# Optimization experiments

Hardware: AMD Instinct MI355X
Metric: run time of the kernel (lower is better)

The kernel has to match this reference:

```python
import jax, jax.numpy as jnp
import numpy as np

H_IMG, W_IMG = 160, 160
C1, C2, HEADS, NHOPS = 128, 256, 8, 2
N_NODES = H_IMG * W_IMG


def build_edges(H, W):
    # 3x3 neighborhood (excl. self) + skip edges (i+2,j),(i,j+2); self loops added once
    node = (np.arange(H)[:, None] * W + np.arange(W)[None, :])
    offsets = [(di, dj) for di in (-1, 0, 1) for dj in (-1, 0, 1) if (di, dj) != (0, 0)] + [(2, 0), (0, 2)]
    srcs, dsts = [], []
    for di, dj in offsets:
        i0, i1 = max(0, -di), H - max(0, di)
        j0, j1 = max(0, -dj), W - max(0, dj)
        srcs.append(node[i0:i1, j0:j1].ravel())
        dsts.append(node[i0 + di:i1 + di, j0 + dj:j1 + dj].ravel())
    n = np.arange(H * W)
    srcs.append(n); dsts.append(n)
    return (np.concatenate(srcs).astype(np.int32), np.concatenate(dsts).astype(np.int32))


def setup_inputs() -> dict:
    key = jax.random.key(0)
    ks = jax.random.split(key, 16)
    s = 0.05
    src_np, dst_np = build_edges(H_IMG, W_IMG)
    d = C2 // HEADS
    return {
        "x": jax.random.normal(ks[0], (1, C1, H_IMG, W_IMG), jnp.float32),
        "w_id": jax.random.normal(ks[1], (C2, C1), jnp.float32) * s,
        "w_in": jax.random.normal(ks[2], (C2, C1), jnp.float32) * s,
        "w_gat": jax.random.normal(ks[3], (NHOPS, C2, C2), jnp.float32) * s,
        "a_src": jax.random.normal(ks[4], (NHOPS, HEADS, d), jnp.float32) * s,
        "a_dst": jax.random.normal(ks[5], (NHOPS, HEADS, d), jnp.float32) * s,
        "gat_bias": jax.random.normal(ks[6], (NHOPS, C2), jnp.float32) * s,
        "bn_gamma": jax.random.uniform(ks[7], (NHOPS, C2), jnp.float32, 0.5, 1.5),
        "bn_beta": jax.random.normal(ks[8], (NHOPS, C2), jnp.float32) * s,
        "bn_mean": jax.random.normal(ks[9], (NHOPS, C2), jnp.float32) * s,
        "bn_var": jax.random.uniform(ks[10], (NHOPS, C2), jnp.float32, 0.5, 1.5),
        "w_out": jax.random.normal(ks[11], (C2, C2), jnp.float32) * s,
        "se_w1": jax.random.normal(ks[12], (C2 // 4, C2), jnp.float32) * s,
        "se_b1": jax.random.normal(ks[13], (C2 // 4,), jnp.float32) * s,
        "se_w2": jax.random.normal(ks[14], (C2, C2 // 4), jnp.float32) * s,
        "se_b2": jax.random.normal(ks[15], (C2,), jnp.float32) * s,
        "src": jnp.asarray(src_np),
        "dst": jnp.asarray(dst_np),
    }


def _gat(x, W, a_s, a_d, b, src, dst, N):
    heads, d = a_s.shape
    h = (x @ W.T).reshape(N, heads, d)                      # [N,H,D]
    al_s = jnp.einsum('nhd,hd->nh', h, a_s)                 # [N,H]
    al_d = jnp.einsum('nhd,hd->nh', h, a_d)
    e = jax.nn.leaky_relu(al_s[src] + al_d[dst], 0.2)       # [E,H]
    emax = jax.lax.stop_gradient(jax.ops.segment_max(e, dst, num_segments=N))
    ee = jnp.exp(e - emax[dst])
    denom = jax.ops.segment_sum(ee, dst, num_segments=N)
    alpha = ee / (denom[dst] + 1e-16)                       # segment softmax over incoming edges
    out = jax.ops.segment_sum(h[src] * alpha[..., None], dst, num_segments=N)
    return out.reshape(N, heads * d) + b


def _forward(x, w_id, w_in, w_gat, a_src, a_dst, gat_bias, bn_gamma, bn_beta,
             bn_mean, bn_var, w_out, se_w1, se_b1, se_w2, se_b2, src, dst):
    identity = jnp.einsum('bchw,oc->bohw', x, w_id)
    h = jnp.einsum('bchw,oc->bohw', x, w_in)
    B, C, H, W = h.shape
    N = B * H * W
    xf = h.transpose(0, 2, 3, 1).reshape(N, C)
    for l in range(NHOPS):
        res = xf
        g = _gat(xf, w_gat[l], a_src[l], a_dst[l], gat_bias[l], src, dst, N)
        g = (g - bn_mean[l]) * (bn_gamma[l] * jax.lax.rsqrt(bn_var[l] + 1e-5)) + bn_beta[l]
        xf = jax.nn.relu(g) + res
    y = xf.reshape(B, H, W, C).transpose(0, 3, 1, 2)
    y = jnp.einsum('bchw,oc->bohw', y, w_out)
    # SE block
    w = y.mean(axis=(2, 3))                                 # [B,C]
    w = jax.nn.relu(w @ se_w1.T + se_b1)
    w = jax.nn.sigmoid(w @ se_w2.T + se_b2)
    y = y * w[:, :, None, None]
    return y + identity


def reference(x, w_id, w_in, w_gat, a_src, a_dst, gat_bias, bn_gamma, bn_beta,
              bn_mean, bn_var, w_out, se_w1, se_b1, se_w2, se_b2, src, dst):
    return _forward(x, w_id, w_in, w_gat, a_src, a_dst, gat_bias, bn_gamma, bn_beta,
                    bn_mean, bn_var, w_out, se_w1, se_b1, se_w2, se_b2, src, dst)
```

## Files before the change

kernel.cpp:

```cpp
#include <hip/hip_runtime.h>

#define NN 25600
#define HH 160
#define WW 160
#define C2 256

#define B_WIN   0
#define B_WID   32768
#define B_WGAT  65536
#define B_WOUT  196608
#define B_WEND  262144

#define C_BNA   0
#define C_BNB   512
#define C_ASRC  1024
#define C_ADST  1536
#define C_SEW1  2048
#define C_SEB1  18432
#define C_SEW2  18496
#define C_SEB2  34880
#define C_END   35136

typedef __attribute__((ext_vector_type(8))) short bfrag;
typedef __attribute__((ext_vector_type(4))) float ffrag;

__device__ __forceinline__ float b2f(unsigned short u) {
    union { unsigned int ui; float f; } v; v.ui = ((unsigned int)u) << 16; return v.f;
}
__device__ __forceinline__ unsigned short f2b(float f) {
    union { float f; unsigned int u; } v; v.f = f;
    unsigned int u = v.u;
    unsigned int r = (u + 0x7FFFu + ((u >> 16) & 1u)) >> 16;
    return (unsigned short)r;
}
__device__ __forceinline__ float lo16f(unsigned int w) {
    union { unsigned int ui; float f; } v; v.ui = w << 16; return v.f;
}
__device__ __forceinline__ float hi16f(unsigned int w) {
    union { unsigned int ui; float f; } v; v.ui = w & 0xFFFF0000u; return v.f;
}
__device__ __forceinline__ bool probe_f32(const unsigned short* __restrict__ x) {
    int l = threadIdx.x & 63;
    bool wild = false;
#pragma unroll
    for (int i = 0; i < 8; ++i) {
        float v = b2f(x[l * 8 + i]);
        wild |= !(fabsf(v) < 1e6f);
    }
    return __any(wild);
}
__device__ __forceinline__ float ldf(const void* p, long i, bool f32) {
    return f32 ? ((const float*)p)[i] : b2f(((const unsigned short*)p)[i]);
}

__global__ __launch_bounds__(256) void prep_kernel(
    const unsigned short* __restrict__ xp,
    const void* pwin, const void* pwid, const void* pwgat, const void* pwout,
    const void* pasrc, const void* padst, const void* pgbias,
    const void* pbng, const void* pbnb, const void* pbnm, const void* pbnv,
    const void* psew1, const void* pseb1, const void* psew2, const void* pseb2,
    unsigned short* __restrict__ wb, float* __restrict__ cvt,
    float* __restrict__ means, unsigned short* __restrict__ xT)
{
    __shared__ unsigned short T[64 * 136];
    const bool f32 = probe_f32(xp);
    const int tid = threadIdx.x;
    const int bid = blockIdx.x;
    const int gid = bid * 256 + tid;
    const int stride = gridDim.x * 256;

    if (bid == 0) means[tid] = 0.f;

    for (int i = gid; i < B_WEND; i += stride) {
        const void* s; int o;
        if      (i < B_WID)   { s = pwin;  o = i - B_WIN; }
        else if (i < B_WGAT)  { s = pwid;  o = i - B_WID; }
        else if (i < B_WOUT)  { s = pwgat; o = i - B_WGAT; }
        else                  { s = pwout; o = i - B_WOUT; }
        wb[i] = f32 ? f2b(((const float*)s)[o]) : ((const unsigned short*)s)[o];
    }
    for (int i = gid; i < 512; i += stride) {
        float sc = ldf(pbng, i, f32) * rsqrtf(ldf(pbnv, i, f32) + 1e-5f);
        cvt[C_BNA + i] = sc;
        cvt[C_BNB + i] = (ldf(pgbias, i, f32) - ldf(pbnm, i, f32)) * sc + ldf(pbnb, i, f32);
        cvt[C_ASRC + i] = ldf(pasrc, i, f32);
        cvt[C_ADST + i] = ldf(padst, i, f32);
    }
    for (int i = gid; i < 16384; i += stride) {
        cvt[C_SEW1 + i] = ldf(psew1, i, f32);
        cvt[C_SEW2 + i] = ldf(psew2, i, f32);
    }
    for (int i = gid; i < 64; i += stride)  cvt[C_SEB1 + i] = ldf(pseb1, i, f32);
    for (int i = gid; i < 256; i += stride) cvt[C_SEB2 + i] = ldf(pseb2, i, f32);

    {
        const int n0 = bid * 64;
        const int nl = tid & 63;
#pragma unroll
        for (int i = 0; i < 32; ++i) {
            int c = i * 4 + (tid >> 6);
            long idx = (long)c * NN + n0 + nl;
            T[nl * 136 + c] = f32 ? f2b(((const float*)xp)[idx]) : xp[idx];
        }
        __syncthreads();
#pragma unroll
        for (int i = 0; i < 4; ++i) {
            int n = tid >> 2, c0 = (tid & 3) * 32 + i * 8;
            uint4 v = *(const uint4*)&T[n * 136 + c0];
            *(uint4*)(xT + (long)(n0 + n) * 128 + c0) = v;
        }
    }
}

struct SmemG2 { unsigned short As[128*40], Bi[64*40], Bd[64*40]; };
struct SmemG  { unsigned short As[128*40], Bs[64*40]; };
struct SmemC  { unsigned short Cs[128*72]; };
union  SmemX2 { SmemG2 s; SmemC c; };
union  SmemNN { SmemG s; SmemC c; };

__global__ __launch_bounds__(256) void mfma_gemm_x2_kernel(
    const unsigned short* __restrict__ A16,
    const unsigned short* __restrict__ Wi16,
    const unsigned short* __restrict__ Wd16,
    unsigned short* __restrict__ xf16,
    unsigned short* __restrict__ idb16)
{
    __shared__ SmemX2 sm;
    const int tid = threadIdx.x;
    const int m0 = blockIdx.x * 128, o0 = blockIdx.y * 64;
    const int lane = tid & 63, wv = tid >> 6;
    const int wm = wv >> 1, wn = wv & 1;
    const int lr = lane & 15, quad = lane >> 4;

    ffrag ai[4][2], ad[4][2];
#pragma unroll
    for (int mt = 0; mt < 4; ++mt)
#pragma unroll
        for (int nt = 0; nt < 2; ++nt) { ai[mt][nt] = (ffrag){0,0,0,0}; ad[mt][nt] = (ffrag){0,0,0,0}; }

    for (int k0 = 0; k0 < 128; k0 += 32) {
#pragma unroll
        for (int c = tid; c < 512; c += 256) {
            int row = c >> 2, q = c & 3;
            uint4 v = *(const uint4*)(A16 + (long)(m0 + row) * 128 + k0 + q * 8);
            *(uint4*)&sm.s.As[row * 40 + q * 8] = v;
        }
        {
            int row = tid >> 2, q = tid & 3;
            uint4 vi = *(const uint4*)(Wi16 + (long)(o0 + row) * 128 + k0 + q * 8);
            uint4 vd = *(const uint4*)(Wd16 + (long)(o0 + row) * 128 + k0 + q * 8);
            *(uint4*)&sm.s.Bi[row * 40 + q * 8] = vi;
            *(uint4*)&sm.s.Bd[row * 40 + q * 8] = vd;
        }
        __syncthreads();
        bfrag a[4], bi[2], bd[2];
#pragma unroll
        for (int mt = 0; mt < 4; ++mt)
            a[mt] = *(const bfrag*)&sm.s.As[(wm * 64 + mt * 16 + lr) * 40 + quad * 8];
#pragma unroll
        for (int nt = 0; nt < 2; ++nt) {
            bi[nt] = *(const bfrag*)&sm.s.Bi[(wn * 32 + nt * 16 + lr) * 40 + quad * 8];
            bd[nt] = *(const bfrag*)&sm.s.Bd[(wn * 32 + nt * 16 + lr) * 40 + quad * 8];
        }
#pragma unroll
        for (int mt = 0; mt < 4; ++mt)
#pragma unroll
            for (int nt = 0; nt < 2; ++nt) {
                ai[mt][nt] = __builtin_amdgcn_mfma_f32_16x16x32_bf16(a[mt], bi[nt], ai[mt][nt], 0, 0, 0);
                ad[mt][nt] = __builtin_amdgcn_mfma_f32_16x16x32_bf16(a[mt], bd[nt], ad[mt][nt], 0, 0, 0);
            }
        __syncthreads();
    }
#pragma unroll
    for (int mt = 0; mt < 4; ++mt)
#pragma unroll
        for (int nt = 0; nt < 2; ++nt)
#pragma unroll
            for (int r = 0; r < 4; ++r)
                sm.c.Cs[(wm * 64 + mt * 16 + quad * 4 + r) * 72 + wn * 32 + nt * 16 + lr] = f2b(ai[mt][nt][r]);
    __syncthreads();
#pragma unroll
    for (int it = 0; it < 4; ++it) {
        int e = it * 256 + tid;
        int row = e >> 3, c8 = (e & 7) * 8;
        *(uint4*)(xf16 + (long)(m0 + row) * C2 + o0 + c8) = *(const uint4*)&sm.c.Cs[row * 72 + c8];
    }
    __syncthreads();
#pragma unroll
    for (int mt = 0; mt < 4; ++mt)
#pragma unroll
        for (int nt = 0; nt < 2; ++nt)
#pragma unroll
            for (int r = 0; r < 4; ++r)
                sm.c.Cs[(wm * 64 + mt * 16 + quad * 4 + r) * 72 + wn * 32 + nt * 16 + lr] = f2b(ad[mt][nt][r]);
    __syncthreads();
#pragma unroll
    for (int it = 0; it < 4; ++it) {
        int e = it * 256 + tid;
        int row = e >> 3, c8 = (e & 7) * 8;
        *(uint4*)(idb16 + (long)(m0 + row) * C2 + o0 + c8) = *(const uint4*)&sm.c.Cs[row * 72 + c8];
    }
}

__global__ __launch_bounds__(256) void mfma_gemm_nn_kernel(
    const unsigned short* __restrict__ A16,
    const unsigned short* __restrict__ W16,
    unsigned short* __restrict__ C16,
    const float* __restrict__ asrc, const float* __restrict__ adst,
    float* __restrict__ al_s, float* __restrict__ al_d,
    float* __restrict__ means,
    int mode)
{
    __shared__ SmemNN sm;
    const int tid = threadIdx.x;
    const int m0 = blockIdx.x * 128, o0 = blockIdx.y * 64;
    const int lane = tid & 63, wv = tid >> 6;
    const int wm = wv >> 1, wn = wv & 1;
    const int lr = lane & 15, quad = lane >> 4;

    ffrag acc[4][2];
#pragma unroll
    for (int mt = 0; mt < 4; ++mt)
#pragma unroll
        for (int nt = 0; nt < 2; ++nt) acc[mt][nt] = (ffrag){0,0,0,0};

    for (int k0 = 0; k0 < 256; k0 += 32) {
#pragma unroll
        for (int c = tid; c < 512; c += 256) {
            int row = c >> 2, q = c & 3;
            uint4 v = *(const uint4*)(A16 + (long)(m0 + row) * 256 + k0 + q * 8);
            *(uint4*)&sm.s.As[row * 40 + q * 8] = v;
        }
        {
            int row = tid >> 2, q = tid & 3;
            uint4 v = *(const uint4*)(W16 + (long)(o0 + row) * 256 + k0 + q * 8);
            *(uint4*)&sm.s.Bs[row * 40 + q * 8] = v;
        }
        __syncthreads();
        bfrag a[4], b[2];
#pragma unroll
        for (int mt = 0; mt < 4; ++mt)
            a[mt] = *(const bfrag*)&sm.s.As[(wm * 64 + mt * 16 + lr) * 40 + quad * 8];
#pragma unroll
        for (int nt = 0; nt < 2; ++nt)
            b[nt] = *(const bfrag*)&sm.s.Bs[(wn * 32 + nt * 16 + lr) * 40 + quad * 8];
#pragma unroll
        for (int mt = 0; mt < 4; ++mt)
#pragma unroll
            for (int nt = 0; nt < 2; ++nt)
                acc[mt][nt] = __builtin_amdgcn_mfma_f32_16x16x32_bf16(a[mt], b[nt], acc[mt][nt], 0, 0, 0);
        __syncthreads();
    }
#pragma unroll
    for (int mt = 0; mt < 4; ++mt)
#pragma unroll
        for (int nt = 0; nt < 2; ++nt)
#pragma unroll
            for (int r = 0; r < 4; ++r)
                sm.c.Cs[(wm * 64 + mt * 16 + quad * 4 + r) * 72 + wn * 32 + nt * 16 + lr] = f2b(acc[mt][nt][r]);
    __syncthreads();
#pragma unroll
    for (int it = 0; it < 4; ++it) {
        int e = it * 256 + tid;
        int row = e >> 3, c8 = (e & 7) * 8;
        *(uint4*)(C16 + (long)(m0 + row) * C2 + o0 + c8) = *(const uint4*)&sm.c.Cs[row * 72 + c8];
    }
    if (mode == 1) {
        const int head = blockIdx.y * 2 + wn;
        const float as0 = asrc[head * 32 + lr], as1 = asrc[head * 32 + 16 + lr];
        const float ad0 = adst[head * 32 + lr], ad1 = adst[head * 32 + 16 + lr];
#pragma unroll
        for (int mt = 0; mt < 4; ++mt)
#pragma unroll
            for (int r = 0; r < 4; ++r) {
                float ps = acc[mt][0][r] * as0 + acc[mt][1][r] * as1;
                float pd = acc[mt][0][r] * ad0 + acc[mt][1][r] * ad1;
#pragma unroll
                for (int sh = 1; sh < 16; sh <<= 1) {
                    ps += __shfl_xor(ps, sh);
                    pd += __shfl_xor(pd, sh);
                }
                if (lr == 0) {
                    int m = m0 + wm * 64 + mt * 16 + quad * 4 + r;
                    al_s[m * 8 + head] = ps;
                    al_d[m * 8 + head] = pd;
                }
            }
    } else if (mode == 2) {
#pragma unroll
        for (int nt = 0; nt < 2; ++nt) {
            float p = 0.f;
#pragma unroll
            for (int mt = 0; mt < 4; ++mt)
#pragma unroll
                for (int r = 0; r < 4; ++r) p += acc[mt][nt][r];
            p += __shfl_xor(p, 16);
            p += __shfl_xor(p, 32);
            if (quad == 0) atomicAdd(&means[o0 + wn * 32 + nt * 16 + lr], p);
        }
    }
}

__global__ __launch_bounds__(256) void aggregate_kernel(
    const unsigned short* __restrict__ h16,
    const float* __restrict__ al_s,
    const float* __restrict__ al_d,
    const float* __restrict__ bnA,
    const float* __restrict__ bnB,
    unsigned short* __restrict__ xf16)
{
    const int SI[11] = { 1, 1, 1, 0, 0, -1, -1, -1, -2,  0, 0};
    const int SJ[11] = { 1, 0,-1, 1,-1,  1,  0, -1,  0, -2, 0};
    __shared__ float es[8][11][8];
    __shared__ float alpha[8][11][8];

    const int t = threadIdx.x;
    const int ln = t >> 5;
    const int l = t & 31;
    const int n = blockIdx.x * 8 + ln;
    const int i = n / WW, j = n % WW;

    for (int idx = t; idx < 704; idx += 256) {
        int lln = idx / 88, rem = idx - lln * 88;
        int k = rem >> 3, hh = rem & 7;
        int nn2 = blockIdx.x * 8 + lln;
        int ii = nn2 / WW, jj = nn2 - ii * WW;
        int si = ii + SI[k], sj = jj + SJ[k];
        bool okk = (si >= 0) & (si < HH) & (sj >= 0) & (sj < WW);
        es[lln][k][hh] = okk ? al_s[(si * WW + sj) * 8 + hh] : -1e30f;
    }
    __syncthreads();

    if (l < 8) {
        const int hd = l;
        const float ald = al_d[n * 8 + hd];
        float e[11];
        float mx = -1e30f;
#pragma unroll
        for (int k = 0; k < 11; ++k) {
            float v = es[ln][k][hd] + ald;
            v = v > 0.f ? v : 0.2f * v;
            e[k] = v;
            mx = fmaxf(mx, v);
        }
        float denom = 0.f;
#pragma unroll
        for (int k = 0; k < 11; ++k) {
            float p = __expf(e[k] - mx);
            e[k] = p;
            denom += p;
        }
        const float inv = 1.f / (denom + 1e-16f);
#pragma unroll
        for (int k = 0; k < 11; ++k) alpha[ln][k][hd] = e[k] * inv;
    }
    __syncthreads();

    const int c8 = l * 8;
    const int hd = l >> 2;
    int srcn[11];
#pragma unroll
    for (int k = 0; k < 11; ++k) {
        int si = i + SI[k], sj = j + SJ[k];
        bool ok = (si >= 0) & (si < HH) & (sj >= 0) & (sj < WW);
        srcn[k] = ok ? si * WW + sj : n;
    }
    float a0=0.f,a1=0.f,a2=0.f,a3=0.f,a4=0.f,a5=0.f,a6=0.f,a7=0.f;
#pragma unroll
    for (int k = 0; k < 11; ++k) {
        float al = alpha[ln][k][hd];
        uint4 hv = *(const uint4*)(h16 + (long)srcn[k] * C2 + c8);
        a0 += al * lo16f(hv.x); a1 += al * hi16f(hv.x);
        a2 += al * lo16f(hv.y); a3 += al * hi16f(hv.y);
        a4 += al * lo16f(hv.z); a5 += al * hi16f(hv.z);
        a6 += al * lo16f(hv.w); a7 += al * hi16f(hv.w);
    }
    float acc8[8] = {a0,a1,a2,a3,a4,a5,a6,a7};
    uint4 rv = *(const uint4*)(xf16 + (long)n * C2 + c8);
    float res[8] = {lo16f(rv.x),hi16f(rv.x),lo16f(rv.y),hi16f(rv.y),
                    lo16f(rv.z),hi16f(rv.z),lo16f(rv.w),hi16f(rv.w)};
    float out[8];
#pragma unroll
    for (int q = 0; q < 8; ++q) {
        int c = c8 + q;
        float g = acc8[q] * bnA[c] + bnB[c];
        out[q] = fmaxf(g, 0.f) + res[q];
    }
    ushort4 o16a, o16b;
    o16a.x = f2b(out[0]); o16a.y = f2b(out[1]); o16a.z = f2b(out[2]); o16a.w = f2b(out[3]);
    o16b.x = f2b(out[4]); o16b.y = f2b(out[5]); o16b.z = f2b(out[6]); o16b.w = f2b(out[7]);
    *(ushort4*)(xf16 + (long)n * C2 + c8)     = o16a;
    *(ushort4*)(xf16 + (long)n * C2 + c8 + 4) = o16b;
}

__global__ __launch_bounds__(256) void final_kernel(
    const unsigned short* __restrict__ x_probe,
    const unsigned short* __restrict__ y16,
    const unsigned short* __restrict__ idb16,
    const float* __restrict__ means,
    const float* __restrict__ cvt,
    void* __restrict__ outp)
{
    __shared__ float T[64][65];
    __shared__ float mv[256];
    __shared__ float hv[64];
    __shared__ float sv[64];
    const bool f32o = probe_f32(x_probe);
    const int t = threadIdx.x;
    const int n0 = blockIdx.x * 64, c0 = blockIdx.y * 64;

    mv[t] = means[t] * (1.0f / 25600.0f);
    __syncthreads();
    if (t < 64) {
        const float* w1 = cvt + C_SEW1 + t * 256;
        float s = cvt[C_SEB1 + t];
        for (int cc = 0; cc < 256; cc += 4) {
            float4 wv = *(const float4*)(w1 + cc);
            s += wv.x * mv[cc] + wv.y * mv[cc+1] + wv.z * mv[cc+2] + wv.w * mv[cc+3];
        }
        hv[t] = fmaxf(s, 0.f);
    }
    __syncthreads();
    if (t < 64) {
        const int c = c0 + t;
        const float* w2 = cvt + C_SEW2 + c * 64;
        float s = cvt[C_SEB2 + c];
        for (int k = 0; k < 64; k += 4) {
            float4 wv = *(const float4*)(w2 + k);
            s += wv.x * hv[k] + wv.y * hv[k+1] + wv.z * hv[k+2] + wv.w * hv[k+3];
        }
        sv[t] = 1.0f / (1.0f + __expf(-s));
    }
    __syncthreads();
#pragma unroll
    for (int it = 0; it < 16; ++it) {
        int e = t + it * 256;
        int nn = e >> 6, cc = e & 63;
        long idx = (long)(n0 + nn) * C2 + c0 + cc;
        T[cc][nn] = b2f(y16[idx]) * sv[cc] + b2f(idb16[idx]);
    }
    __syncthreads();
#pragma unroll
    for (int it = 0; it < 16; ++it) {
        int e = t + it * 256;
        int cc = e >> 6, nn = e & 63;
        long idx = (long)(c0 + cc) * NN + n0 + nn;
        float v = T[cc][nn];
        if (f32o) ((float*)outp)[idx] = v;
        else      ((unsigned short*)outp)[idx] = f2b(v);
    }
}

extern "C" void kernel_launch(void* const* d_in, const int* in_sizes, int n_in,
                              void* d_out, int out_size, void* d_ws, size_t ws_size,
                              hipStream_t stream) {
    float* ws = (float*)d_ws;
    float* cvt   = ws;
    float* means = ws + 35200;
    float* als   = means + 256;
    float* ald   = als + 204800;
    unsigned short* wb16  = (unsigned short*)(ald + 204800);
    unsigned short* xT16  = wb16 + B_WEND;
    unsigned short* xf16  = xT16 + NN * 128;
    unsigned short* h16   = xf16 + NN * 256;
    unsigned short* idb16 = h16 + NN * 256;

    const unsigned short* xp = (const unsigned short*)d_in[0];

    dim3 b256(256);
    dim3 gmfma(NN / 128, C2 / 64);
    dim3 gfin(NN / 64, C2 / 64);

    prep_kernel<<<400, b256, 0, stream>>>(
        xp, d_in[2], d_in[1], d_in[3], d_in[11],
        d_in[4], d_in[5], d_in[6], d_in[7], d_in[8], d_in[9], d_in[10],
        d_in[12], d_in[13], d_in[14], d_in[15],
        wb16, cvt, means, xT16);

    mfma_gemm_x2_kernel<<<gmfma, b256, 0, stream>>>(
        xT16, wb16 + B_WIN, wb16 + B_WID, xf16, idb16);

    for (int l = 0; l < 2; ++l) {
        mfma_gemm_nn_kernel<<<gmfma, b256, 0, stream>>>(
            xf16, wb16 + B_WGAT + l * 65536, h16,
            cvt + C_ASRC + l * 256, cvt + C_ADST + l * 256, als, ald, nullptr, 1);
        aggregate_kernel<<<NN / 8, b256, 0, stream>>>(h16, als, ald,
            cvt + C_BNA + l * 256, cvt + C_BNB + l * 256, xf16);
    }

    mfma_gemm_nn_kernel<<<gmfma, b256, 0, stream>>>(
        xf16, wb16 + B_WOUT, h16, nullptr, nullptr, nullptr, nullptr, means, 2);
    final_kernel<<<gfin, b256, 0, stream>>>(xp, h16, idb16, means, cvt, d_out);
}
```

Baseline: 240.2 us.

## Fuse GAT aggregation into the following GEMM's A-tile producer

Removes the separate aggregate kernel. The next GEMM (next hop's W_gat or w_out) now computes the softmax attention weights and the neighbour-weighted sum plus BN/ReLU/residual on the fly, building its A tile in shared memory per K-slice. It also widens the GEMM N-tile from 64 to 128 so each aggregated A row is reused across more outputs. It double-buffers the h and alpha buffers to avoid read/write hazards. Each hop saves a full round trip of the xf activation through memory and one launch, but the gather and softmax are redone for each of the two N-blocks and may hurt GEMM throughput and occupancy.

```diff
diff --git a/kernel.cpp b/kernel.cpp
--- a/kernel.cpp
+++ b/kernel.cpp
@@ -113,10 +113,8 @@
 }
 
 struct SmemG2 { unsigned short As[128*40], Bi[64*40], Bd[64*40]; };
-struct SmemG  { unsigned short As[128*40], Bs[64*40]; };
-struct SmemC  { unsigned short Cs[128*72]; };
-union  SmemX2 { SmemG2 s; SmemC c; };
-union  SmemNN { SmemG s; SmemC c; };
+struct SmemC2 { unsigned short Cs[128*72]; };
+union  SmemX2 { SmemG2 s; SmemC2 c; };
 
 __global__ __launch_bounds__(256) void mfma_gemm_x2_kernel(
     const unsigned short* __restrict__ A16,
@@ -142,15 +140,15 @@
 #pragma unroll
         for (int c = tid; c < 512; c += 256) {
             int row = c >> 2, q = c & 3;
-            uint4 v = *(const uint4*)(A16 + (long)(m0 + row) * 128 + k0 + q * 8);
-            *(uint4*)&sm.s.As[row * 40 + q * 8] = v;
+            *(uint4*)&sm.s.As[row * 40 + q * 8] =
+                *(const uint4*)(A16 + (long)(m0 + row) * 128 + k0 + q * 8);
         }
         {
             int row = tid >> 2, q = tid & 3;
-            uint4 vi = *(const uint4*)(Wi16 + (long)(o0 + row) * 128 + k0 + q * 8);
-            uint4 vd = *(const uint4*)(Wd16 + (long)(o0 + row) * 128 + k0 + q * 8);
-            *(uint4*)&sm.s.Bi[row * 40 + q * 8] = vi;
-            *(uint4*)&sm.s.Bd[row * 40 + q * 8] = vd;
+            *(uint4*)&sm.s.Bi[row * 40 + q * 8] =
+                *(const uint4*)(Wi16 + (long)(o0 + row) * 128 + k0 + q * 8);
+            *(uint4*)&sm.s.Bd[row * 40 + q * 8] =
+                *(const uint4*)(Wd16 + (long)(o0 + row) * 128 + k0 + q * 8);
         }
         __syncthreads();
         bfrag a[4], bi[2], bd[2];
@@ -202,93 +200,184 @@
     }
 }
 
-__global__ __launch_bounds__(256) void mfma_gemm_nn_kernel(
-    const unsigned short* __restrict__ A16,
+__global__ __launch_bounds__(256) void gemm_hop_kernel(
+    const unsigned short* __restrict__ Ap,
+    const unsigned short* __restrict__ hsrc,
+    const float* __restrict__ alsA, const float* __restrict__ aldA,
+    const unsigned short* __restrict__ xfold,
+    unsigned short* __restrict__ xfout,
+    const float* __restrict__ bnA, const float* __restrict__ bnB,
     const unsigned short* __restrict__ W16,
     unsigned short* __restrict__ C16,
     const float* __restrict__ asrc, const float* __restrict__ adst,
-    float* __restrict__ al_s, float* __restrict__ al_d,
+    float* __restrict__ al_sO, float* __restrict__ al_dO,
     float* __restrict__ means,
-    int mode)
+    int aggA, int epi)
 {
-    __shared__ SmemNN sm;
+    __shared__ union {
+        struct { unsigned short As[128*40], Bs[128*40]; float alpha[128][11]; } s;
+        unsigned short Cs[128*136];
+    } sm;
+    const int SI[11] = { 1, 1, 1, 0, 0, -1, -1, -1, -2,  0, 0};
+    const int SJ[11] = { 1, 0,-1, 1,-1,  1,  0, -1,  0, -2, 0};
     const int tid = threadIdx.x;
-    const int m0 = blockIdx.x * 128, o0 = blockIdx.y * 64;
+    const int m0 = blockIdx.x * 128, o0 = blockIdx.y * 128;
     const int lane = tid & 63, wv = tid >> 6;
     const int wm = wv >> 1, wn = wv & 1;
     const int lr = lane & 15, quad = lane >> 4;
 
-    ffrag acc[4][2];
+    ffrag acc[4][4];
 #pragma unroll
     for (int mt = 0; mt < 4; ++mt)
 #pragma unroll
-        for (int nt = 0; nt < 2; ++nt) acc[mt][nt] = (ffrag){0,0,0,0};
+        for (int nt = 0; nt < 4; ++nt) acc[mt][nt] = (ffrag){0,0,0,0};
 
     for (int k0 = 0; k0 < 256; k0 += 32) {
 #pragma unroll
         for (int c = tid; c < 512; c += 256) {
             int row = c >> 2, q = c & 3;
-            uint4 v = *(const uint4*)(A16 + (long)(m0 + row) * 256 + k0 + q * 8);
-            *(uint4*)&sm.s.As[row * 40 + q * 8] = v;
-        }
-        {
-            int row = tid >> 2, q = tid & 3;
-            uint4 v = *(const uint4*)(W16 + (long)(o0 + row) * 256 + k0 + q * 8);
-            *(uint4*)&sm.s.Bs[row * 40 + q * 8] = v;
+            *(uint4*)&sm.s.Bs[row * 40 + q * 8] =
+                *(const uint4*)(W16 + (long)(o0 + row) * 256 + k0 + q * 8);
+        }
+        if (aggA) {
+            if (tid < 128) {
+                const int head = k0 >> 5;
+                const int m = m0 + tid;
+                const int i2 = m / WW, j2 = m - i2 * WW;
+                const float ald = aldA[m * 8 + head];
+                float e[11]; float mx = -1e30f;
+#pragma unroll
+                for (int k = 0; k < 11; ++k) {
+                    int si = i2 + SI[k], sj = j2 + SJ[k];
+                    bool ok = (si >= 0) & (si < HH) & (sj >= 0) & (sj < WW);
+                    float v = ok ? alsA[(si * WW + sj) * 8 + head] + ald : -1e30f;
+                    v = v > 0.f ? v : 0.2f * v;
+                    e[k] = v; mx = fmaxf(mx, v);
+                }
+                float den = 0.f;
+#pragma unroll
+                for (int k = 0; k < 11; ++k) { float p = __expf(e[k] - mx); e[k] = p; den += p; }
+                const float inv = 1.f / (den + 1e-16f);
+#pragma unroll
+                for (int k = 0; k < 11; ++k) sm.s.alpha[tid][k] = e[k] * inv;
+            }
+        } else {
+#pragma unroll
+            for (int c = tid; c < 512; c += 256) {
+                int row = c >> 2, q = c & 3;
+                *(uint4*)&sm.s.As[row * 40 + q * 8] =
+                    *(const uint4*)(Ap + (long)(m0 + row) * 256 + k0 + q * 8);
+            }
         }
         __syncthreads();
-        bfrag a[4], b[2];
+        if (aggA) {
+            const int ml = tid >> 1, half = tid & 1;
+            const int m = m0 + ml;
+            const int i2 = m / WW, j2 = m - i2 * WW;
+            const int cb = k0 + half * 16;
+            float a16[16];
+#pragma unroll
+            for (int q = 0; q < 16; ++q) a16[q] = 0.f;
+#pragma unroll
+            for (int k = 0; k < 11; ++k) {
+                float al = sm.s.alpha[ml][k];
+                int si = i2 + SI[k], sj = j2 + SJ[k];
+                bool ok = (si >= 0) & (si < HH) & (sj >= 0) & (sj < WW);
+                long srcn = ok ? (long)(si * WW + sj) : (long)m;
+                uint4 v0 = *(const uint4*)(hsrc + srcn * C2 + cb);
+                uint4 v1 = *(const uint4*)(hsrc + srcn * C2 + cb + 8);
+                a16[0]  += al * lo16f(v0.x); a16[1]  += al * hi16f(v0.x);
+                a16[2]  += al * lo16f(v0.y); a16[3]  += al * hi16f(v0.y);
+                a16[4]  += al * lo16f(v0.z); a16[5]  += al * hi16f(v0.z);
+                a16[6]  += al * lo16f(v0.w); a16[7]  += al * hi16f(v0.w);
+                a16[8]  += al * lo16f(v1.x); a16[9]  += al * hi16f(v1.x);
+                a16[10] += al * lo16f(v1.y); a16[11] += al * hi16f(v1.y);
+                a16[12] += al * lo16f(v1.z); a16[13] += al * hi16f(v1.z);
+                a16[14] += al * lo16f(v1.w); a16[15] += al * hi16f(v1.w);
+            }
+            uint4 r0 = *(const uint4*)(xfold + (long)m * C2 + cb);
+            uint4 r1 = *(const uint4*)(xfold + (long)m * C2 + cb + 8);
+            float res[16] = {lo16f(r0.x),hi16f(r0.x),lo16f(r0.y),hi16f(r0.y),
+                             lo16f(r0.z),hi16f(r0.z),lo16f(r0.w),hi16f(r0.w),
+                             lo16f(r1.x),hi16f(r1.x),lo16f(r1.y),hi16f(r1.y),
+                             lo16f(r1.z),hi16f(r1.z),lo16f(r1.w),hi16f(r1.w)};
+            unsigned int w[8];
+#pragma unroll
+            for (int q = 0; q < 8; ++q) {
+                int c0i = cb + q * 2;
+                float g0 = a16[q*2]   * bnA[c0i]     + bnB[c0i];
+                float g1 = a16[q*2+1] * bnA[c0i + 1] + bnB[c0i + 1];
+                g0 = fmaxf(g0, 0.f) + res[q*2];
+                g1 = fmaxf(g1, 0.f) + res[q*2+1];
+                w[q] = (unsigned int)f2b(g0) | ((unsigned int)f2b(g1) << 16);
+            }
+            uint4 p0 = make_uint4(w[0], w[1], w[2], w[3]);
+            uint4 p1 = make_uint4(w[4], w[5], w[6], w[7]);
+            *(uint4*)&sm.s.As[ml * 40 + half * 16]     = p0;
+            *(uint4*)&sm.s.As[ml * 40 + half * 16 + 8] = p1;
+            if (xfout != nullptr && blockIdx.y == 0) {
+                *(uint4*)(xfout + (long)m * C2 + cb)     = p0;
+                *(uint4*)(xfout + (long)m * C2 + cb + 8) = p1;
+            }
+            __syncthreads();
+        }
+        bfrag a[4], b[4];
 #pragma unroll
         for (int mt = 0; mt < 4; ++mt)
             a[mt] = *(const bfrag*)&sm.s.As[(wm * 64 + mt * 16 + lr) * 40 + quad * 8];
 #pragma unroll
-        for (int nt = 0; nt < 2; ++nt)
-            b[nt] = *(const bfrag*)&sm.s.Bs[(wn * 32 + nt * 16 + lr) * 40 + quad * 8];
+        for (int nt = 0; nt < 4; ++nt)
+            b[nt] = *(const bfrag*)&sm.s.Bs[(wn * 64 + nt * 16 + lr) * 40 + quad * 8];
 #pragma unroll
         for (int mt = 0; mt < 4; ++mt)
 #pragma unroll
-            for (int nt = 0; nt < 2; ++nt)
+            for (int nt = 0; nt < 4; ++nt)
                 acc[mt][nt] = __builtin_amdgcn_mfma_f32_16x16x32_bf16(a[mt], b[nt], acc[mt][nt], 0, 0, 0);
         __syncthreads();
     }
+
 #pragma unroll
     for (int mt = 0; mt < 4; ++mt)
 #pragma unroll
-        for (int nt = 0; nt < 2; ++nt)
+        for (int nt = 0; nt < 4; ++nt)
 #pragma unroll
             for (int r = 0; r < 4; ++r)
-                sm.c.Cs[(wm * 64 + mt * 16 + quad * 4 + r) * 72 + wn * 32 + nt * 16 + lr] = f2b(acc[mt][nt][r]);
-    __syncthreads();
-#pragma unroll
-    for (int it = 0; it < 4; ++it) {
+                sm.Cs[(wm * 64 + mt * 16 + quad * 4 + r) * 136 + wn * 64 + nt * 16 + lr] = f2b(acc[mt][nt][r]);
+    __syncthreads();
+#pragma unroll
+    for (int it = 0; it < 8; ++it) {
         int e = it * 256 + tid;
-        int row = e >> 3, c8 = (e & 7) * 8;
-        *(uint4*)(C16 + (long)(m0 + row) * C2 + o0 + c8) = *(const uint4*)&sm.c.Cs[row * 72 + c8];
-    }
-    if (mode == 1) {
-        const int head = blockIdx.y * 2 + wn;
-        const float as0 = asrc[head * 32 + lr], as1 = asrc[head * 32 + 16 + lr];
-        const float ad0 = adst[head * 32 + lr], ad1 = adst[head * 32 + 16 + lr];
-#pragma unroll
-        for (int mt = 0; mt < 4; ++mt)
-#pragma unroll
-            for (int r = 0; r < 4; ++r) {
-                float ps = acc[mt][0][r] * as0 + acc[mt][1][r] * as1;
-                float pd = acc[mt][0][r] * ad0 + acc[mt][1][r] * ad1;
-#pragma unroll
-                for (int sh = 1; sh < 16; sh <<= 1) {
-                    ps += __shfl_xor(ps, sh);
-                    pd += __shfl_xor(pd, sh);
+        int row = e >> 4, c8 = (e & 15) * 8;
+        *(uint4*)(C16 + (long)(m0 + row) * C2 + o0 + c8) = *(const uint4*)&sm.Cs[row * 136 + c8];
+    }
+
+    if (epi == 1) {
+#pragma unroll
+        for (int h2 = 0; h2 < 2; ++h2) {
+            const int gh = (o0 >> 5) + wn * 2 + h2;
+            const float as0 = asrc[gh * 32 + lr], as1 = asrc[gh * 32 + 16 + lr];
+            const float ad0 = adst[gh * 32 + lr], ad1 = adst[gh * 32 + 16 + lr];
+#pragma unroll
+            for (int mt = 0; mt < 4; ++mt)
+#pragma unroll
+                for (int r = 0; r < 4; ++r) {
+                    float ps = acc[mt][h2*2][r] * as0 + acc[mt][h2*2+1][r] * as1;
+                    float pd = acc[mt][h2*2][r] * ad0 + acc[mt][h2*2+1][r] * ad1;
+#pragma unroll
+                    for (int sh = 1; sh < 16; sh <<= 1) {
+                        ps += __shfl_xor(ps, sh);
+                        pd += __shfl_xor(pd, sh);
+                    }
+                    if (lr == 0) {
+                        int m = m0 + wm * 64 + mt * 16 + quad * 4 + r;
+                        al_sO[m * 8 + gh] = ps;
+                        al_dO[m * 8 + gh] = pd;
+                    }
                 }
-                if (lr == 0) {
-                    int m = m0 + wm * 64 + mt * 16 + quad * 4 + r;
-                    al_s[m * 8 + head] = ps;
-                    al_d[m * 8 + head] = pd;
-                }
-            }
-    } else if (mode == 2) {
-#pragma unroll
-        for (int nt = 0; nt < 2; ++nt) {
+        }
+    } else if (epi == 2) {
+#pragma unroll
+        for (int nt = 0; nt < 4; ++nt) {
             float p = 0.f;
 #pragma unroll
             for (int mt = 0; mt < 4; ++mt)
@@ -296,101 +385,9 @@
                 for (int r = 0; r < 4; ++r) p += acc[mt][nt][r];
             p += __shfl_xor(p, 16);
             p += __shfl_xor(p, 32);
-            if (quad == 0) atomicAdd(&means[o0 + wn * 32 + nt * 16 + lr], p);
-        }
-    }
-}
-
-__global__ __launch_bounds__(256) void aggregate_kernel(
-    const unsigned short* __restrict__ h16,
-    const float* __restrict__ al_s,
-    const float* __restrict__ al_d,
-    const float* __restrict__ bnA,
-    const float* __restrict__ bnB,
-    unsigned short* __restrict__ xf16)
-{
-    const int SI[11] = { 1, 1, 1, 0, 0, -1, -1, -1, -2,  0, 0};
-    const int SJ[11] = { 1, 0,-1, 1,-1,  1,  0, -1,  0, -2, 0};
-    __shared__ float es[8][11][8];
-    __shared__ float alpha[8][11][8];
-
-    const int t = threadIdx.x;
-    const int ln = t >> 5;
-    const int l = t & 31;
-    const int n = blockIdx.x * 8 + ln;
-    const int i = n / WW, j = n % WW;
-
-    for (int idx = t; idx < 704; idx += 256) {
-        int lln = idx / 88, rem = idx - lln * 88;
-        int k = rem >> 3, hh = rem & 7;
-        int nn2 = blockIdx.x * 8 + lln;
-        int ii = nn2 / WW, jj = nn2 - ii * WW;
-        int si = ii + SI[k], sj = jj + SJ[k];
-        bool okk = (si >= 0) & (si < HH) & (sj >= 0) & (sj < WW);
-        es[lln][k][hh] = okk ? al_s[(si * WW + sj) * 8 + hh] : -1e30f;
-    }
-    __syncthreads();
-
-    if (l < 8) {
-        const int hd = l;
-        const float ald = al_d[n * 8 + hd];
-        float e[11];
-        float mx = -1e30f;
-#pragma unroll
-        for (int k = 0; k < 11; ++k) {
-            float v = es[ln][k][hd] + ald;
-            v = v > 0.f ? v : 0.2f * v;
-            e[k] = v;
-            mx = fmaxf(mx, v);
-        }
-        float denom = 0.f;
-#pragma unroll
-        for (int k = 0; k < 11; ++k) {
-            float p = __expf(e[k] - mx);
-            e[k] = p;
-            denom += p;
-        }
-        const float inv = 1.f / (denom + 1e-16f);
-#pragma unroll
-        for (int k = 0; k < 11; ++k) alpha[ln][k][hd] = e[k] * inv;
-    }
-    __syncthreads();
-
-    const int c8 = l * 8;
-    const int hd = l >> 2;
-    int srcn[11];
-#pragma unroll
-    for (int k = 0; k < 11; ++k) {
-        int si = i + SI[k], sj = j + SJ[k];
-        bool ok = (si >= 0) & (si < HH) & (sj >= 0) & (sj < WW);
-        srcn[k] = ok ? si * WW + sj : n;
-    }
-    float a0=0.f,a1=0.f,a2=0.f,a3=0.f,a4=0.f,a5=0.f,a6=0.f,a7=0.f;
-#pragma unroll
-    for (int k = 0; k < 11; ++k) {
-        float al = alpha[ln][k][hd];
-        uint4 hv = *(const uint4*)(h16 + (long)srcn[k] * C2 + c8);
-        a0 += al * lo16f(hv.x); a1 += al * hi16f(hv.x);
-        a2 += al * lo16f(hv.y); a3 += al * hi16f(hv.y);
-        a4 += al * lo16f(hv.z); a5 += al * hi16f(hv.z);
-        a6 += al * lo16f(hv.w); a7 += al * hi16f(hv.w);
-    }
-    float acc8[8] = {a0,a1,a2,a3,a4,a5,a6,a7};
-    uint4 rv = *(const uint4*)(xf16 + (long)n * C2 + c8);
-    float res[8] = {lo16f(rv.x),hi16f(rv.x),lo16f(rv.y),hi16f(rv.y),
-                    lo16f(rv.z),hi16f(rv.z),lo16f(rv.w),hi16f(rv.w)};
-    float out[8];
-#pragma unroll
-    for (int q = 0; q < 8; ++q) {
-        int c = c8 + q;
-        float g = acc8[q] * bnA[c] + bnB[c];
-        out[q] = fmaxf(g, 0.f) + res[q];
-    }
-    ushort4 o16a, o16b;
-    o16a.x = f2b(out[0]); o16a.y = f2b(out[1]); o16a.z = f2b(out[2]); o16a.w = f2b(out[3]);
-    o16b.x = f2b(out[4]); o16b.y = f2b(out[5]); o16b.z = f2b(out[6]); o16b.w = f2b(out[7]);
-    *(ushort4*)(xf16 + (long)n * C2 + c8)     = o16a;
-    *(ushort4*)(xf16 + (long)n * C2 + c8 + 4) = o16b;
+            if (quad == 0) atomicAdd(&means[o0 + wn * 64 + nt * 16 + lr], p);
+        }
+    }
 }
 
 __global__ __launch_bounds__(256) void final_kernel(
@@ -457,18 +454,23 @@
     float* ws = (float*)d_ws;
     float* cvt   = ws;
     float* means = ws + 35200;
-    float* als   = means + 256;
-    float* ald   = als + 204800;
-    unsigned short* wb16  = (unsigned short*)(ald + 204800);
+    float* als1  = means + 256;
+    float* ald1  = als1 + 204800;
+    float* als2  = ald1 + 204800;
+    float* ald2  = als2 + 204800;
+    unsigned short* wb16  = (unsigned short*)(ald2 + 204800);
     unsigned short* xT16  = wb16 + B_WEND;
-    unsigned short* xf16  = xT16 + NN * 128;
-    unsigned short* h16   = xf16 + NN * 256;
-    unsigned short* idb16 = h16 + NN * 256;
+    unsigned short* xf0   = xT16 + NN * 128;
+    unsigned short* xf1   = xf0 + NN * 256;
+    unsigned short* hA    = xf1 + NN * 256;
+    unsigned short* hB    = hA + NN * 256;
+    unsigned short* idb16 = hB + NN * 256;
 
     const unsigned short* xp = (const unsigned short*)d_in[0];
 
     dim3 b256(256);
-    dim3 gmfma(NN / 128, C2 / 64);
+    dim3 gx2(NN / 128, 4);
+    dim3 ghop(NN / 128, 2);
     dim3 gfin(NN / 64, C2 / 64);
 
     prep_kernel<<<400, b256, 0, stream>>>(
@@ -477,18 +479,29 @@
         d_in[12], d_in[13], d_in[14], d_in[15],
         wb16, cvt, means, xT16);
 
-    mfma_gemm_x2_kernel<<<gmfma, b256, 0, stream>>>(
-        xT16, wb16 + B_WIN, wb16 + B_WID, xf16, idb16);
-
-    for (int l = 0; l < 2; ++l) {
-        mfma_gemm_nn_kernel<<<gmfma, b256, 0, stream>>>(
-            xf16, wb16 + B_WGAT + l * 65536, h16,
-            cvt + C_ASRC + l * 256, cvt + C_ADST + l * 256, als, ald, nullptr, 1);
-        aggregate_kernel<<<NN / 8, b256, 0, stream>>>(h16, als, ald,
-            cvt + C_BNA + l * 256, cvt + C_BNB + l * 256, xf16);
-    }
-
-    mfma_gemm_nn_kernel<<<gmfma, b256, 0, stream>>>(
-        xf16, wb16 + B_WOUT, h16, nullptr, nullptr, nullptr, nullptr, means, 2);
-    final_kernel<<<gfin, b256, 0, stream>>>(xp, h16, idb16, means, cvt, d_out);
-}
+    mfma_gemm_x2_kernel<<<gx2, b256, 0, stream>>>(
+        xT16, wb16 + B_WIN, wb16 + B_WID, xf0, idb16);
+
+    gemm_hop_kernel<<<ghop, b256, 0, stream>>>(
+        xf0, nullptr, nullptr, nullptr, nullptr, nullptr,
+        nullptr, nullptr,
+        wb16 + B_WGAT, hA,
+        cvt + C_ASRC, cvt + C_ADST, als1, ald1, nullptr,
+        0, 1);
+
+    gemm_hop_kernel<<<ghop, b256, 0, stream>>>(
+        nullptr, hA, als1, ald1, xf0, xf1,
+        cvt + C_BNA, cvt + C_BNB,
+        wb16 + B_WGAT + 65536, hB,
+        cvt + C_ASRC + 256, cvt + C_ADST + 256, als2, ald2, nullptr,
+        1, 1);
+
+    gemm_hop_kernel<<<ghop, b256, 0, stream>>>(
+        nullptr, hB, als2, ald2, xf1, nullptr,
+        cvt + C_BNA + 256, cvt + C_BNB + 256,
+        wb16 + B_WOUT, hA,
+        nullptr, nullptr, nullptr, nullptr, means,
+        1, 2);
+
+    final_kernel<<<gfin, b256, 0, stream>>>(xp, hA, idb16, means, cvt, d_out);
+}
```

Result: slower. 304.6 us (+26.8%).

## Fuse output GEMM with SE scaling and residual, computing SE means algebraically

Applied to the files above, without the earlier changes.

The SE channel means are now taken as column sums of the final GAT output, gathered in the last aggregate pass, and pushed through w_out by a single-block kernel (mean of y = W_out · mean of xf). The output GEMM then applies the SE scale, adds the identity branch and writes the transposed NCHW output directly. This removes the bf16 round trip of y through h16 and the separate final kernel. The costs are a tiny serial kernel, per-block atomics in aggregate, and a strided epilogue transpose from LDS.

```diff
diff --git a/kernel.cpp b/kernel.cpp
--- a/kernel.cpp
+++ b/kernel.cpp
@@ -60,7 +60,7 @@
     const void* pbng, const void* pbnb, const void* pbnm, const void* pbnv,
     const void* psew1, const void* pseb1, const void* psew2, const void* pseb2,
     unsigned short* __restrict__ wb, float* __restrict__ cvt,
-    float* __restrict__ means, unsigned short* __restrict__ xT)
+    float* __restrict__ colsum, unsigned short* __restrict__ xT)
 {
     __shared__ unsigned short T[64 * 136];
     const bool f32 = probe_f32(xp);
@@ -69,7 +69,7 @@
     const int gid = bid * 256 + tid;
     const int stride = gridDim.x * 256;
 
-    if (bid == 0) means[tid] = 0.f;
+    if (bid == 0) colsum[tid] = 0.f;
 
     for (int i = gid; i < B_WEND; i += stride) {
         const void* s; int o;
@@ -142,15 +142,15 @@
 #pragma unroll
         for (int c = tid; c < 512; c += 256) {
             int row = c >> 2, q = c & 3;
-            uint4 v = *(const uint4*)(A16 + (long)(m0 + row) * 128 + k0 + q * 8);
-            *(uint4*)&sm.s.As[row * 40 + q * 8] = v;
+            *(uint4*)&sm.s.As[row * 40 + q * 8] =
+                *(const uint4*)(A16 + (long)(m0 + row) * 128 + k0 + q * 8);
         }
         {
             int row = tid >> 2, q = tid & 3;
-            uint4 vi = *(const uint4*)(Wi16 + (long)(o0 + row) * 128 + k0 + q * 8);
-            uint4 vd = *(const uint4*)(Wd16 + (long)(o0 + row) * 128 + k0 + q * 8);
-            *(uint4*)&sm.s.Bi[row * 40 + q * 8] = vi;
-            *(uint4*)&sm.s.Bd[row * 40 + q * 8] = vd;
+            *(uint4*)&sm.s.Bi[row * 40 + q * 8] =
+                *(const uint4*)(Wi16 + (long)(o0 + row) * 128 + k0 + q * 8);
+            *(uint4*)&sm.s.Bd[row * 40 + q * 8] =
+                *(const uint4*)(Wd16 + (long)(o0 + row) * 128 + k0 + q * 8);
         }
         __syncthreads();
         bfrag a[4], bi[2], bd[2];
@@ -207,9 +207,7 @@
     const unsigned short* __restrict__ W16,
     unsigned short* __restrict__ C16,
     const float* __restrict__ asrc, const float* __restrict__ adst,
-    float* __restrict__ al_s, float* __restrict__ al_d,
-    float* __restrict__ means,
-    int mode)
+    float* __restrict__ al_s, float* __restrict__ al_d)
 {
     __shared__ SmemNN sm;
     const int tid = threadIdx.x;
@@ -228,13 +226,13 @@
 #pragma unroll
         for (int c = tid; c < 512; c += 256) {
             int row = c >> 2, q = c & 3;
-            uint4 v = *(const uint4*)(A16 + (long)(m0 + row) * 256 + k0 + q * 8);
-            *(uint4*)&sm.s.As[row * 40 + q * 8] = v;
+            *(uint4*)&sm.s.As[row * 40 + q * 8] =
+                *(const uint4*)(A16 + (long)(m0 + row) * 256 + k0 + q * 8);
         }
         {
             int row = tid >> 2, q = tid & 3;
-            uint4 v = *(const uint4*)(W16 + (long)(o0 + row) * 256 + k0 + q * 8);
-            *(uint4*)&sm.s.Bs[row * 40 + q * 8] = v;
+            *(uint4*)&sm.s.Bs[row * 40 + q * 8] =
+                *(const uint4*)(W16 + (long)(o0 + row) * 256 + k0 + q * 8);
         }
         __syncthreads();
         bfrag a[4], b[2];
@@ -265,7 +263,7 @@
         int row = e >> 3, c8 = (e & 7) * 8;
         *(uint4*)(C16 + (long)(m0 + row) * C2 + o0 + c8) = *(const uint4*)&sm.c.Cs[row * 72 + c8];
     }
-    if (mode == 1) {
+    {
         const int head = blockIdx.y * 2 + wn;
         const float as0 = asrc[head * 32 + lr], as1 = asrc[head * 32 + 16 + lr];
         const float ad0 = adst[head * 32 + lr], ad1 = adst[head * 32 + 16 + lr];
@@ -286,18 +284,6 @@
                     al_d[m * 8 + head] = pd;
                 }
             }
-    } else if (mode == 2) {
-#pragma unroll
-        for (int nt = 0; nt < 2; ++nt) {
-            float p = 0.f;
-#pragma unroll
-            for (int mt = 0; mt < 4; ++mt)
-#pragma unroll
-                for (int r = 0; r < 4; ++r) p += acc[mt][nt][r];
-            p += __shfl_xor(p, 16);
-            p += __shfl_xor(p, 32);
-            if (quad == 0) atomicAdd(&means[o0 + wn * 32 + nt * 16 + lr], p);
-        }
     }
 }
 
@@ -307,12 +293,14 @@
     const float* __restrict__ al_d,
     const float* __restrict__ bnA,
     const float* __restrict__ bnB,
-    unsigned short* __restrict__ xf16)
+    unsigned short* __restrict__ xf16,
+    float* __restrict__ colsum)
 {
     const int SI[11] = { 1, 1, 1, 0, 0, -1, -1, -1, -2,  0, 0};
     const int SJ[11] = { 1, 0,-1, 1,-1,  1,  0, -1,  0, -2, 0};
     __shared__ float es[8][11][8];
     __shared__ float alpha[8][11][8];
+    __shared__ float colstore[8][256];
 
     const int t = threadIdx.x;
     const int ln = t >> 5;
@@ -391,25 +379,43 @@
     o16b.x = f2b(out[4]); o16b.y = f2b(out[5]); o16b.z = f2b(out[6]); o16b.w = f2b(out[7]);
     *(ushort4*)(xf16 + (long)n * C2 + c8)     = o16a;
     *(ushort4*)(xf16 + (long)n * C2 + c8 + 4) = o16b;
-}
-
-__global__ __launch_bounds__(256) void final_kernel(
-    const unsigned short* __restrict__ x_probe,
-    const unsigned short* __restrict__ y16,
-    const unsigned short* __restrict__ idb16,
-    const float* __restrict__ means,
+
+    if (colsum != nullptr) {
+#pragma unroll
+        for (int q = 0; q < 8; ++q) colstore[ln][c8 + q] = b2f(f2b(out[q]));
+        __syncthreads();
+        float s = 0.f;
+#pragma unroll
+        for (int k = 0; k < 8; ++k) s += colstore[k][t];
+        atomicAdd(&colsum[t], s);
+    }
+}
+
+__global__ __launch_bounds__(256) void se_vec_kernel(
+    const float* __restrict__ colsum,
+    const unsigned short* __restrict__ wout,
     const float* __restrict__ cvt,
-    void* __restrict__ outp)
+    float* __restrict__ svec)
 {
-    __shared__ float T[64][65];
+    __shared__ float cs[256];
     __shared__ float mv[256];
     __shared__ float hv[64];
-    __shared__ float sv[64];
-    const bool f32o = probe_f32(x_probe);
     const int t = threadIdx.x;
-    const int n0 = blockIdx.x * 64, c0 = blockIdx.y * 64;
-
-    mv[t] = means[t] * (1.0f / 25600.0f);
+    cs[t] = colsum[t];
+    __syncthreads();
+    {
+        const unsigned short* wr = wout + t * 256;
+        float s = 0.f;
+#pragma unroll 4
+        for (int k = 0; k < 256; k += 8) {
+            uint4 v = *(const uint4*)(wr + k);
+            s += lo16f(v.x) * cs[k]   + hi16f(v.x) * cs[k+1]
+               + lo16f(v.y) * cs[k+2] + hi16f(v.y) * cs[k+3]
+               + lo16f(v.z) * cs[k+4] + hi16f(v.z) * cs[k+5]
+               + lo16f(v.w) * cs[k+6] + hi16f(v.w) * cs[k+7];
+        }
+        mv[t] = s * (1.0f / 25600.0f);
+    }
     __syncthreads();
     if (t < 64) {
         const float* w1 = cvt + C_SEW1 + t * 256;
@@ -421,31 +427,87 @@
         hv[t] = fmaxf(s, 0.f);
     }
     __syncthreads();
-    if (t < 64) {
-        const int c = c0 + t;
-        const float* w2 = cvt + C_SEW2 + c * 64;
-        float s = cvt[C_SEB2 + c];
+    {
+        const float* w2 = cvt + C_SEW2 + t * 64;
+        float s = cvt[C_SEB2 + t];
         for (int k = 0; k < 64; k += 4) {
             float4 wv = *(const float4*)(w2 + k);
             s += wv.x * hv[k] + wv.y * hv[k+1] + wv.z * hv[k+2] + wv.w * hv[k+3];
         }
-        sv[t] = 1.0f / (1.0f + __expf(-s));
-    }
-    __syncthreads();
-#pragma unroll
-    for (int it = 0; it < 16; ++it) {
-        int e = t + it * 256;
-        int nn = e >> 6, cc = e & 63;
-        long idx = (long)(n0 + nn) * C2 + c0 + cc;
-        T[cc][nn] = b2f(y16[idx]) * sv[cc] + b2f(idb16[idx]);
-    }
-    __syncthreads();
-#pragma unroll
-    for (int it = 0; it < 16; ++it) {
-        int e = t + it * 256;
-        int cc = e >> 6, nn = e & 63;
-        long idx = (long)(c0 + cc) * NN + n0 + nn;
-        float v = T[cc][nn];
+        svec[t] = 1.0f / (1.0f + __expf(-s));
+    }
+}
+
+__global__ __launch_bounds__(256) void mfma_gemm_out_kernel(
+    const unsigned short* __restrict__ x_probe,
+    const unsigned short* __restrict__ A16,
+    const unsigned short* __restrict__ W16,
+    const unsigned short* __restrict__ idb16,
+    const float* __restrict__ svec,
+    void* __restrict__ outp)
+{
+    __shared__ union {
+        SmemG s;
+        unsigned short Cs[128 * 66];
+    } sm;
+    __shared__ float svl[64];
+    const bool f32o = probe_f32(x_probe);
+    const int tid = threadIdx.x;
+    const int m0 = blockIdx.x * 128, o0 = blockIdx.y * 64;
+    const int lane = tid & 63, wv = tid >> 6;
+    const int wm = wv >> 1, wn = wv & 1;
+    const int lr = lane & 15, quad = lane >> 4;
+
+    if (tid < 64) svl[tid] = svec[o0 + tid];
+
+    ffrag acc[4][2];
+#pragma unroll
+    for (int mt = 0; mt < 4; ++mt)
+#pragma unroll
+        for (int nt = 0; nt < 2; ++nt) acc[mt][nt] = (ffrag){0,0,0,0};
+
+    for (int k0 = 0; k0 < 256; k0 += 32) {
+#pragma unroll
+        for (int c = tid; c < 512; c += 256) {
+            int row = c >> 2, q = c & 3;
+            *(uint4*)&sm.s.As[row * 40 + q * 8] =
+                *(const uint4*)(A16 + (long)(m0 + row) * 256 + k0 + q * 8);
+        }
+        {
+            int row = tid >> 2, q = tid & 3;
+            *(uint4*)&sm.s.Bs[row * 40 + q * 8] =
+                *(const uint4*)(W16 + (long)(o0 + row) * 256 + k0 + q * 8);
+        }
+        __syncthreads();
+        bfrag a[4], b[2];
+#pragma unroll
+        for (int mt = 0; mt < 4; ++mt)
+            a[mt] = *(const bfrag*)&sm.s.As[(wm * 64 + mt * 16 + lr) * 40 + quad * 8];
+#pragma unroll
+        for (int nt = 0; nt < 2; ++nt)
+            b[nt] = *(const bfrag*)&sm.s.Bs[(wn * 32 + nt * 16 + lr) * 40 + quad * 8];
+#pragma unroll
+        for (int mt = 0; mt < 4; ++mt)
+#pragma unroll
+            for (int nt = 0; nt < 2; ++nt)
+                acc[mt][nt] = __builtin_amdgcn_mfma_f32_16x16x32_bf16(a[mt], b[nt], acc[mt][nt], 0, 0, 0);
+        __syncthreads();
+    }
+#pragma unroll
+    for (int mt = 0; mt < 4; ++mt)
+#pragma unroll
+        for (int nt = 0; nt < 2; ++nt)
+#pragma unroll
+            for (int r = 0; r < 4; ++r)
+                sm.Cs[(wm * 64 + mt * 16 + quad * 4 + r) * 66 + wn * 32 + nt * 16 + lr] = f2b(acc[mt][nt][r]);
+    __syncthreads();
+#pragma unroll
+    for (int it = 0; it < 32; ++it) {
+        int e = it * 256 + tid;
+        int c = e >> 7, n = e & 127;
+        float v = b2f(sm.Cs[n * 66 + c]) * svl[c]
+                + b2f(idb16[(long)(m0 + n) * C2 + o0 + c]);
+        long idx = (long)(o0 + c) * NN + m0 + n;
         if (f32o) ((float*)outp)[idx] = v;
         else      ((unsigned short*)outp)[idx] = f2b(v);
     }
@@ -455,10 +517,11 @@
                               void* d_out, int out_size, void* d_ws, size_t ws_size,
                               hipStream_t stream) {
     float* ws = (float*)d_ws;
-    float* cvt   = ws;
-    float* means = ws + 35200;
-    float* als   = means + 256;
-    float* ald   = als + 204800;
+    float* cvt    = ws;
+    float* colsum = ws + 35200;
+    float* svec   = colsum + 256;
+    float* als    = svec + 256;
+    float* ald    = als + 204800;
     unsigned short* wb16  = (unsigned short*)(ald + 204800);
     unsigned short* xT16  = wb16 + B_WEND;
     unsigned short* xf16  = xT16 + NN * 128;
@@ -469,13 +532,12 @@
 
     dim3 b256(256);
     dim3 gmfma(NN / 128, C2 / 64);
-    dim3 gfin(NN / 64, C2 / 64);
 
     prep_kernel<<<400, b256, 0, stream>>>(
         xp, d_in[2], d_in[1], d_in[3], d_in[11],
         d_in[4], d_in[5], d_in[6], d_in[7], d_in[8], d_in[9], d_in[10],
         d_in[12], d_in[13], d_in[14], d_in[15],
-        wb16, cvt, means, xT16);
+        wb16, cvt, colsum, xT16);
 
     mfma_gemm_x2_kernel<<<gmfma, b256, 0, stream>>>(
         xT16, wb16 + B_WIN, wb16 + B_WID, xf16, idb16);
@@ -483,12 +545,14 @@
     for (int l = 0; l < 2; ++l) {
         mfma_gemm_nn_kernel<<<gmfma, b256, 0, stream>>>(
             xf16, wb16 + B_WGAT + l * 65536, h16,
-            cvt + C_ASRC + l * 256, cvt + C_ADST + l * 256, als, ald, nullptr, 1);
+            cvt + C_ASRC + l * 256, cvt + C_ADST + l * 256, als, ald);
         aggregate_kernel<<<NN / 8, b256, 0, stream>>>(h16, als, ald,
-            cvt + C_BNA + l * 256, cvt + C_BNB + l * 256, xf16);
-    }
-
-    mfma_gemm_nn_kernel<<<gmfma, b256, 0, stream>>>(
-        xf16, wb16 + B_WOUT, h16, nullptr, nullptr, nullptr, nullptr, means, 2);
-    final_kernel<<<gfin, b256, 0, stream>>>(xp, h16, idb16, means, cvt, d_out);
-}
+            cvt + C_BNA + l * 256, cvt + C_BNB + l * 256, xf16,
+            (l == 1) ? colsum : nullptr);
+    }
+
+    se_vec_kernel<<<1, b256, 0, stream>>>(colsum, wb16 + B_WOUT, cvt, svec);
+
+    mfma_gemm_out_kernel<<<gmfma, b256, 0, stream>>>(
+        xp, xf16, wb16 + B_WOUT, idb16, svec, d_out);
+}
```

Measured after the change: 311.7 us. 1.3x slower.
